# Optimization experiments

Measured on AMD Instinct MI355X. Metric: run time of the kernel, lower is better.

## Reference

```python
import jax, jax.numpy as jnp
import numpy as np

THRESH = 0.7


def setup_inputs() -> dict:
    key = jax.random.key(0)
    k1, k2, k3 = jax.random.split(key, 3)
    B, A, H, W = 16, 9, 128, 128
    cla_map = jax.random.normal(k1, (B, 2 * A, H, W), dtype=jnp.float32)
    reg_map = jax.random.normal(k2, (B, 4 * A, H, W), dtype=jnp.float32)
    anchor = jax.random.uniform(k3, (H * W * A, 6), dtype=jnp.float32)
    return {"cla_map": cla_map, "reg_map": reg_map, "anchor": anchor,
            "src_info": 2048, "num_anchors": A}


def reference(cla_map, reg_map, anchor, src_info, num_anchors):
    B, _, H, W = cla_map.shape
    A = num_anchors
    S = float(src_info)

    # per-anchor 2-way softmax foreground score: channels are anchor-major pairs
    cla = cla_map.reshape(B, A, 2, H, W)
    fg = jax.nn.softmax(cla, axis=2)[:, :, 1]          # [B, A, H, W]

    # anchor lookup replicates original index: anchor[(k*W + k) * p]
    k_idx = jnp.arange(W)
    p_idx = jnp.arange(A)
    idx = (k_idx[None, :] * W + k_idx[None, :]) * p_idx[:, None]   # [A, W]
    anc = anchor[idx]                                   # [A, W, 6]
    acx = anc[..., 2][None, :, None, :]                 # -> broadcast [B,A,H,W]
    acy = anc[..., 3][None, :, None, :]
    aw = anc[..., 4][None, :, None, :]
    ah = anc[..., 5][None, :, None, :]

    # box decode (embedding): meta -> absolute cx,cy,w,h in source-image pixels
    reg = reg_map.reshape(B, A, 4, H, W)
    tx, ty, tw, th = reg[:, :, 0], reg[:, :, 1], reg[:, :, 2], reg[:, :, 3]
    cx = (tx * aw + acx) * S
    cy = (ty * ah + acy) * S
    w = jnp.exp(tw) * aw * S
    h = jnp.exp(th) * ah * S

    # data2box: center/size -> corners
    ltx = cx - w * 0.5
    lty = cy - h * 0.5
    rbx = cx + w * 0.5
    rby = cy + h * 0.5

    # keep boxes with fg > 0.7 that lie fully inside the source image
    valid = (fg > THRESH) & (ltx >= 0) & (lty >= 0) & (rbx <= S) & (rby <= S)
    m = valid.astype(cla_map.dtype)[..., None]          # [B, A, H, W, 1]

    proposal = jnp.stack([ltx, lty, rbx, rby], axis=-1) * m   # [B,A,H,W,4]
    rpn_box = (jnp.stack([cx, cy, w, h], axis=-1) / S) * m    # [B,A,H,W,4]
    # fixed-shape stand-in for the variable-length box lists: boxes + mask
    return jnp.concatenate([proposal, rpn_box, m], axis=-1)   # [B,A,H,W,9]
```

## Files before the change

kernel.cpp:

```cpp
#include <hip/hip_runtime.h>
#include <math.h>

#define NB 16
#define NA 9
#define HW 16384
#define SF 2048.0f

typedef float f32x4 __attribute__((ext_vector_type(4)));

__global__ __launch_bounds__(256) void proposal_sparse_kernel(
    const float* __restrict__ cla,
    const float* __restrict__ reg,
    const float* __restrict__ anchor,
    float* __restrict__ out)
{
    const float invS = 1.0f / 2048.0f;

    const int tid = threadIdx.x;
    const int blk = blockIdx.x;
    const int ba  = blk >> 4;
    const int sub = blk & 15;
    const int a   = ba % NA;
    const int b   = ba / NA;

    const int hw0 = (sub << 10) + (tid << 2);
    const int w0  = hw0 & 127;

    const float* cb = cla + (((size_t)(b * (2 * NA) + 2 * a)) << 14) + hw0;
    float4 vc0 = *(const float4*)cb;
    float4 vc1 = *(const float4*)(cb + HW);
    const float* rb = reg + (((size_t)(b * (4 * NA) + 4 * a)) << 14) + hw0;
    float4 vtx = *(const float4*)(rb);
    float4 vty = *(const float4*)(rb + HW);
    float4 vtw = *(const float4*)(rb + 2 * HW);
    float4 vth = *(const float4*)(rb + 3 * HW);

    float ACX[4], ACY[4], AW[4], AH[4];
    #pragma unroll
    for (int j = 0; j < 4; ++j) {
        const int row = (w0 + j) * 129 * a;
        const float* p = anchor + (size_t)row * 6;
        float2 u  = *(const float2*)(p + 2);
        float2 vv = *(const float2*)(p + 4);
        ACX[j] = u.x; ACY[j] = u.y; AW[j] = vv.x; AH[j] = vv.y;
    }

    const float C0[4] = {vc0.x, vc0.y, vc0.z, vc0.w};
    const float C1[4] = {vc1.x, vc1.y, vc1.z, vc1.w};
    const float TX[4] = {vtx.x, vtx.y, vtx.z, vtx.w};
    const float TY[4] = {vty.x, vty.y, vty.z, vty.w};
    const float TW[4] = {vtw.x, vtw.y, vtw.z, vtw.w};
    const float TH[4] = {vth.x, vth.y, vth.z, vth.w};

    float v[36];
    int   vmask = 0;

    #pragma unroll
    for (int j = 0; j < 4; ++j) {
        const float c0 = C0[j], c1 = C1[j];
        const float tx = TX[j], ty = TY[j], tw = TW[j], th = TH[j];
        const float acx = ACX[j], acy = ACY[j], aw = AW[j], ah = AH[j];

        float fg = 1.0f / (1.0f + __expf(c0 - c1));
        float ew = __expf(tw);
        float eh = __expf(th);

        float cx  = (tx * aw + acx) * SF;
        float cy  = (ty * ah + acy) * SF;
        float bw  = (ew * aw) * SF;
        float bh  = (eh * ah) * SF;
        float ltx = cx - bw * 0.5f;
        float lty = cy - bh * 0.5f;
        float rbx = cx + bw * 0.5f;
        float rby = cy + bh * 0.5f;

        const float ex = bw * 3e-4f + 1e-2f;
        const float ey = bh * 3e-4f + 1e-2f;
        bool near = (fabsf(fg - 0.7f) < 3e-4f)
                  | (fabsf(ltx) < ex) | (fabsf(lty) < ey)
                  | (fabsf(rbx - SF) < ex) | (fabsf(rby - SF) < ey);
        if (__builtin_expect(near, 0)) {
#pragma clang fp contract(off)
            float mx = fmaxf(c0, c1);
            float e0 = (float)exp((double)(c0 - mx));
            float e1 = (float)exp((double)(c1 - mx));
            fg = e1 / (e0 + e1);
            ew = (float)exp((double)tw);
            eh = (float)exp((double)th);
            cx  = (tx * aw + acx) * SF;
            cy  = (ty * ah + acy) * SF;
            bw  = (ew * aw) * SF;
            bh  = (eh * ah) * SF;
            ltx = cx - bw * 0.5f;
            lty = cy - bh * 0.5f;
            rbx = cx + bw * 0.5f;
            rby = cy + bh * 0.5f;
        }

        bool valid = (fg > 0.7f) & (ltx >= 0.0f) & (lty >= 0.0f)
                   & (rbx <= SF) & (rby <= SF);
        vmask |= (valid ? 1 : 0) << j;

        v[j * 9 + 0] = ltx;
        v[j * 9 + 1] = lty;
        v[j * 9 + 2] = rbx;
        v[j * 9 + 3] = rby;
        v[j * 9 + 4] = cx * invS;
        v[j * 9 + 5] = cy * invS;
        v[j * 9 + 6] = bw * invS;
        v[j * 9 + 7] = bh * invS;
        v[j * 9 + 8] = 1.0f;
    }

    const size_t e0 = (size_t)blk * 1024 + (size_t)tid * 4;
    #pragma unroll
    for (int j = 0; j < 4; ++j) {
        if (vmask & (1 << j)) {
            float* o = out + (e0 + j) * 9;
            #pragma unroll
            for (int k = 0; k < 9; ++k) o[k] = v[j * 9 + k];
        }
    }
}

extern "C" void kernel_launch(void* const* d_in, const int* in_sizes, int n_in,
                              void* d_out, int out_size, void* d_ws, size_t ws_size,
                              hipStream_t stream) {
    const float* cla    = (const float*)d_in[0];
    const float* reg    = (const float*)d_in[1];
    const float* anchor = (const float*)d_in[2];

    hipMemsetAsync(d_out, 0, (size_t)out_size * sizeof(float), stream);

    const int blocks = (NB * NA * HW) / 1024;
    hipLaunchKernelGGL(proposal_sparse_kernel, dim3(blocks), dim3(256), 0, stream,
                       cla, reg, anchor, (float*)d_out);
}
```

Before: 30.39 us.

## Write full output densely via LDS-staged coalesced stores and drop memset

Replaces the zero memset plus sparse masked scattered writes with a dense write of every output element, multiplying values by the validity mask. Each wave stages its results in shared memory and emits coalesced 16-byte nontemporal stores. This removes a separate full-output memset pass and the uncoalesced 9-float writes, at the cost of always writing all output bytes from the kernel.

Result: faster. 26.09 us (-14.2%).

```diff
diff --git a/kernel.cpp b/kernel.cpp
--- a/kernel.cpp
+++ b/kernel.cpp
@@ -8,7 +8,7 @@
 
 typedef float f32x4 __attribute__((ext_vector_type(4)));
 
-__global__ __launch_bounds__(256) void proposal_sparse_kernel(
+__global__ __launch_bounds__(256) void proposal_kernel(
     const float* __restrict__ cla,
     const float* __restrict__ reg,
     const float* __restrict__ anchor,
@@ -16,12 +16,16 @@
 {
     const float invS = 1.0f / 2048.0f;
 
-    const int tid = threadIdx.x;
-    const int blk = blockIdx.x;
-    const int ba  = blk >> 4;
-    const int sub = blk & 15;
-    const int a   = ba % NA;
-    const int b   = ba / NA;
+    __shared__ float ob[4][2304];
+
+    const int tid  = threadIdx.x;
+    const int wv   = tid >> 6;
+    const int lane = tid & 63;
+    const int blk  = blockIdx.x;
+    const int ba   = blk >> 4;
+    const int sub  = blk & 15;
+    const int a    = ba % NA;
+    const int b    = ba / NA;
 
     const int hw0 = (sub << 10) + (tid << 2);
     const int w0  = hw0 & 127;
@@ -53,7 +57,6 @@
     const float TH[4] = {vth.x, vth.y, vth.z, vth.w};
 
     float v[36];
-    int   vmask = 0;
 
     #pragma unroll
     for (int j = 0; j < 4; ++j) {
@@ -99,28 +102,31 @@
 
         bool valid = (fg > 0.7f) & (ltx >= 0.0f) & (lty >= 0.0f)
                    & (rbx <= SF) & (rby <= SF);
-        vmask |= (valid ? 1 : 0) << j;
+        float m = valid ? 1.0f : 0.0f;
 
-        v[j * 9 + 0] = ltx;
-        v[j * 9 + 1] = lty;
-        v[j * 9 + 2] = rbx;
-        v[j * 9 + 3] = rby;
-        v[j * 9 + 4] = cx * invS;
-        v[j * 9 + 5] = cy * invS;
-        v[j * 9 + 6] = bw * invS;
-        v[j * 9 + 7] = bh * invS;
-        v[j * 9 + 8] = 1.0f;
+        v[j * 9 + 0] = ltx * m;
+        v[j * 9 + 1] = lty * m;
+        v[j * 9 + 2] = rbx * m;
+        v[j * 9 + 3] = rby * m;
+        v[j * 9 + 4] = (cx * invS) * m;
+        v[j * 9 + 5] = (cy * invS) * m;
+        v[j * 9 + 6] = (bw * invS) * m;
+        v[j * 9 + 7] = (bh * invS) * m;
+        v[j * 9 + 8] = m;
     }
 
-    const size_t e0 = (size_t)blk * 1024 + (size_t)tid * 4;
+    float* wob = &ob[wv][0];
     #pragma unroll
-    for (int j = 0; j < 4; ++j) {
-        if (vmask & (1 << j)) {
-            float* o = out + (e0 + j) * 9;
-            #pragma unroll
-            for (int k = 0; k < 9; ++k) o[k] = v[j * 9 + k];
-        }
+    for (int k = 0; k < 9; ++k) {
+        f32x4 t = {v[4 * k], v[4 * k + 1], v[4 * k + 2], v[4 * k + 3]};
+        *(f32x4*)&wob[lane * 36 + 4 * k] = t;
     }
+
+    const f32x4* src4 = (const f32x4*)wob;
+    f32x4* dst4 = (f32x4*)(out + (size_t)blk * 9216 + (size_t)wv * 2304);
+    #pragma unroll
+    for (int k = 0; k < 9; ++k)
+        __builtin_nontemporal_store(src4[k * 64 + lane], &dst4[k * 64 + lane]);
 }
 
 extern "C" void kernel_launch(void* const* d_in, const int* in_sizes, int n_in,
@@ -130,9 +136,7 @@
     const float* reg    = (const float*)d_in[1];
     const float* anchor = (const float*)d_in[2];
 
-    hipMemsetAsync(d_out, 0, (size_t)out_size * sizeof(float), stream);
-
     const int blocks = (NB * NA * HW) / 1024;
-    hipLaunchKernelGGL(proposal_sparse_kernel, dim3(blocks), dim3(256), 0, stream,
+    hipLaunchKernelGGL(proposal_kernel, dim3(blocks), dim3(256), 0, stream,
                        cla, reg, anchor, (float*)d_out);
 }
```
